# Kernel tuning notes

Hardware: AMD Instinct MI355X
Metric: run time of the kernel (lower is better)

The kernel has to match this reference:

```python
import jax, jax.numpy as jnp
import numpy as np

D_MODEL = 1024
NUM_HEADS = 16
HEAD_DIM = D_MODEL // NUM_HEADS

def setup_inputs() -> dict:
    key = jax.random.key(0)
    ks = jax.random.split(key, 5)
    B, T = 4, 2048
    x = jax.random.normal(ks[0], (B, T, D_MODEL), dtype=jnp.float32)
    s = 1.0 / np.sqrt(D_MODEL)
    W_qkv = jax.random.normal(ks[1], (D_MODEL, 3 * D_MODEL), dtype=jnp.float32) * s
    b_qkv = jnp.zeros((3 * D_MODEL,), dtype=jnp.float32)
    W_out = jax.random.normal(ks[2], (D_MODEL, D_MODEL), dtype=jnp.float32) * s
    b_out = jnp.zeros((D_MODEL,), dtype=jnp.float32)
    return {"x": x, "W_qkv": W_qkv, "b_qkv": b_qkv, "W_out": W_out, "b_out": b_out}

def reference(x, W_qkv, b_qkv, W_out, b_out):
    B, T, C = x.shape
    H, Dh = NUM_HEADS, HEAD_DIM
    qkv = x @ W_qkv + b_qkv                      # [B,T,3C]
    qkv = qkv.reshape(B, T, 3, H, Dh)
    q = jnp.transpose(qkv[:, :, 0], (0, 2, 1, 3))  # [B,H,T,Dh]
    k = jnp.transpose(qkv[:, :, 1], (0, 2, 1, 3))
    v = jnp.transpose(qkv[:, :, 2], (0, 2, 1, 3))
    scores = jnp.einsum('bhqd,bhkd->bhqk', q, k) / jnp.sqrt(jnp.asarray(Dh, x.dtype))
    weights = jax.nn.softmax(scores, axis=-1)
    out = jnp.einsum('bhqk,bhkd->bhqd', weights, v)  # [B,H,T,Dh]
    out = jnp.transpose(out, (0, 2, 1, 3)).reshape(B, T, C)
    return out @ W_out + b_out
```

## Files before the change

kernel.cpp:

```cpp
#include <hip/hip_runtime.h>
#include <stdint.h>

typedef __bf16 bf16x8 __attribute__((ext_vector_type(8)));
typedef float f32x4 __attribute__((ext_vector_type(4)));
typedef float f32x16 __attribute__((ext_vector_type(16)));

static constexpr int BB = 4, TT = 2048, CC = 1024, HH = 16, DH = 64;
static constexpr int MM = BB * TT;
static constexpr int N1 = 3 * CC;
static constexpr int KK = CC;

__device__ __forceinline__ unsigned short f2bf(float f) {
  uint32_t u = __builtin_bit_cast(uint32_t, f);
  u += 0x7FFFu + ((u >> 16) & 1u);
  return (unsigned short)(u >> 16);
}

__device__ __forceinline__ void async16(const void* g, void* l) {
  __builtin_amdgcn_global_load_lds((const __attribute__((address_space(1))) void*)g,
                                   (__attribute__((address_space(3))) void*)l, 16, 0, 0);
}

__global__ __launch_bounds__(256) void k_cvt(const float* __restrict__ src,
                                             unsigned short* __restrict__ dst) {
  int i = blockIdx.x * 256 + threadIdx.x;
  const float4* s = (const float4*)src + (size_t)i * 2;
  float4 a = s[0], b = s[1];
  union { unsigned short h[8]; uint4 v; } o;
  o.h[0] = f2bf(a.x); o.h[1] = f2bf(a.y); o.h[2] = f2bf(a.z); o.h[3] = f2bf(a.w);
  o.h[4] = f2bf(b.x); o.h[5] = f2bf(b.y); o.h[6] = f2bf(b.z); o.h[7] = f2bf(b.w);
  ((uint4*)dst)[i] = o.v;
}

__global__ __launch_bounds__(256) void k_tcvt(const float* __restrict__ src,
                                              unsigned short* __restrict__ dst,
                                              int R, int C) {
  __shared__ float tile[32][33];
  int tx = threadIdx.x & 31, ty = threadIdx.x >> 5;
  int c0 = blockIdx.x * 32, r0 = blockIdx.y * 32;
#pragma unroll
  for (int i = 0; i < 4; ++i)
    tile[ty + i * 8][tx] = src[(size_t)(r0 + ty + i * 8) * C + c0 + tx];
  __syncthreads();
#pragma unroll
  for (int i = 0; i < 4; ++i)
    dst[(size_t)(c0 + ty + i * 8) * R + r0 + tx] = f2bf(tile[tx][ty + i * 8]);
}

#define LDA4(Ab, mf, ksl) \
  (*(const bf16x8*)&(Ab)[(wm * 128 + (mf) * 16 + l15) * 64 + \
                         ((((ksl) * 4 + l16) ^ (l15 & 7)) * 8)])
#define LDB4(Bb, nf, ksl) \
  (*(const bf16x8*)&(Bb)[(wn * 32 + (nf) * 16 + l15) * 64 + \
                         ((((ksl) * 4 + l16) ^ (l15 & 7)) * 8)])

struct AF8 { bf16x8 a[8]; };

template <int P, bool LOADB>
__device__ __forceinline__ AF8 phase_pre4(const unsigned short* Ab, const unsigned short* Bb,
                                          int wm, int wn, int l15, int l16, bf16x8* bfr) {
  AF8 f;
#pragma unroll
  for (int mf = 0; mf < 4; ++mf) {
    f.a[mf * 2] = LDA4(Ab, P * 4 + mf, 0);
    f.a[mf * 2 + 1] = LDA4(Ab, P * 4 + mf, 1);
  }
  if (LOADB) {
#pragma unroll
    for (int nf = 0; nf < 2; ++nf) {
      bfr[nf * 2] = LDB4(Bb, nf, 0);
      bfr[nf * 2 + 1] = LDB4(Bb, nf, 1);
    }
  }
  return f;
}

template <int P>
__device__ __forceinline__ void phase_mfma4(const AF8& f, const bf16x8* bfr, f32x4 acc[8][2]) {
#pragma unroll
  for (int mf = 0; mf < 4; ++mf)
#pragma unroll
    for (int nf = 0; nf < 2; ++nf) {
      acc[P * 4 + mf][nf] = __builtin_amdgcn_mfma_f32_16x16x32_bf16(
          f.a[mf * 2], bfr[nf * 2], acc[P * 4 + mf][nf], 0, 0, 0);
      acc[P * 4 + mf][nf] = __builtin_amdgcn_mfma_f32_16x16x32_bf16(
          f.a[mf * 2 + 1], bfr[nf * 2 + 1], acc[P * 4 + mf][nf], 0, 0, 0);
    }
}

#define PHASE4(P, AB, BB_, LOADB, STAGES, WAITS)                      \
  { AF8 f_ = phase_pre4<P, LOADB>(AB, BB_, wm, wn, l15, l16, bfr);    \
    STAGES;                                                           \
    WAITS;                                                            \
    __builtin_amdgcn_s_barrier();                                     \
    asm volatile("s_waitcnt lgkmcnt(0)" ::: "memory");                \
    __builtin_amdgcn_sched_barrier(0);                                \
    __builtin_amdgcn_s_setprio(1);                                    \
    phase_mfma4<P>(f_, bfr, acc);                                     \
    __builtin_amdgcn_s_setprio(0);                                    \
    __builtin_amdgcn_s_barrier(); }

template <int MODE, int NBX>
__global__ __launch_bounds__(512, 2) void k_gemm4(
    const unsigned short* __restrict__ A, const unsigned short* __restrict__ Bt,
    const float* __restrict__ bias, int M, int N, int K,
    unsigned short* __restrict__ qo, unsigned short* __restrict__ ko,
    unsigned short* __restrict__ vo, float* __restrict__ fo) {
  __shared__ __attribute__((aligned(16))) unsigned short lds[49152];
  unsigned short* As0 = lds;
  unsigned short* As1 = lds + 16384;
  unsigned short* Bs0 = lds + 32768;
  unsigned short* Bs1 = lds + 40960;

  const int tid = threadIdx.x;
  const int lane = tid & 63;
  const int w = tid >> 6, wm = w >> 2, wn = w & 3;
  const int l15 = lane & 15, l16 = lane >> 4;

  const int q8 = (int)gridDim.x >> 3;
  const int swz = ((int)blockIdx.x & 7) * q8 + ((int)blockIdx.x >> 3);
  const int m0 = (swz / NBX) * 256, n0 = (swz % NBX) * 128;

  f32x4 acc[8][2] = {};

  const int srow = tid >> 3;
  const int sg = ((tid & 7) ^ (srow & 7)) * 8;
  const int dOff = srow * 64 + (tid & 7) * 8;
  const unsigned short* aBase = A + (size_t)(m0 + srow) * K + sg;
  const unsigned short* bBase = Bt + (size_t)(n0 + srow) * K + sg;

#define STAGE_A(dst, kt, h)                                                          \
  { async16(aBase + (size_t)((h) * 128) * K + (kt) * 64, (dst) + (h) * 8192 + dOff); \
    async16(aBase + (size_t)((h) * 128 + 64) * K + (kt) * 64,                        \
            (dst) + (h) * 8192 + 4096 + dOff); }
#define STAGE_B(dst, kt)                                                             \
  { async16(bBase + (kt) * 64, (dst) + dOff);                                        \
    async16(bBase + (size_t)64 * K + (kt) * 64, (dst) + 4096 + dOff); }

  STAGE_A(As0, 0, 0); STAGE_A(As0, 0, 1);
  STAGE_B(Bs0, 0);
  STAGE_B(Bs1, 1);
  asm volatile("s_waitcnt vmcnt(0)" ::: "memory");
  __builtin_amdgcn_s_barrier();

  const int NITER = K / 128;
#pragma unroll 1
  for (int i = 0; i < NITER; ++i) {
    const bool more = (i + 1 < NITER);
    const int tb = 2 * i + 1, t2k = 2 * i + 2, t3 = 2 * i + 3;
    bf16x8 bfr[4];
    PHASE4(0, As0, Bs0, true,
           { STAGE_A(As1, tb, 0); STAGE_A(As1, tb, 1); }, ((void)0));
    PHASE4(1, As0, Bs0, false,
           { if (more) STAGE_B(Bs0, t2k); },
           { if (more) { asm volatile("s_waitcnt vmcnt(2)" ::: "memory"); }
             else      { asm volatile("s_waitcnt vmcnt(0)" ::: "memory"); } });
    PHASE4(0, As1, Bs1, true,
           { if (more) { STAGE_A(As0, t2k, 0); STAGE_A(As0, t2k, 1); } }, ((void)0));
    PHASE4(1, As1, Bs1, false,
           { if (more) STAGE_B(Bs1, t3); },
           { if (more) { asm volatile("s_waitcnt vmcnt(2)" ::: "memory"); } });
  }

  if (MODE == 0) {
    const int sel = n0 >> 10;
    if (sel < 2) {
      const float qs = (sel == 0) ? 0.180336892f : 1.0f;
      float bj[2];
#pragma unroll
      for (int nf = 0; nf < 2; ++nf) bj[nf] = bias[n0 + wn * 32 + nf * 16 + l15];
#pragma unroll
      for (int mf = 0; mf < 8; ++mf)
#pragma unroll
        for (int nf = 0; nf < 2; ++nf)
#pragma unroll
          for (int r = 0; r < 4; ++r) {
            const int row = wm * 128 + mf * 16 + l16 * 4 + r;
            const int col = wn * 32 + nf * 16 + l15;
            lds[row * 128 + (col >> 6) * 64 +
                ((((col >> 3) & 7) ^ (row & 7)) * 8) + (col & 7)] =
                f2bf((acc[mf][nf][r] + bj[nf]) * qs);
          }
      __syncthreads();
      const int row = tid >> 1, half = tid & 1;
      const int gm = m0 + row, bb2 = gm >> 11, t2 = gm & 2047;
      const int h2 = ((n0 & 1023) >> 6) + half;
      unsigned short* dst = (sel == 0 ? qo : ko) +
          ((size_t)(bb2 * HH + h2) * TT + t2) * DH;
#pragma unroll
      for (int g = 0; g < 8; ++g) {
        bf16x8 v = *(const bf16x8*)&lds[row * 128 + half * 64 + ((g ^ (row & 7)) * 8)];
        *(bf16x8*)&dst[g * 8] = v;
      }
    } else {
#pragma unroll
      for (int mf = 0; mf < 8; ++mf)
#pragma unroll
        for (int nf = 0; nf < 2; ++nf) {
          const int gn = n0 + wn * 32 + nf * 16 + l15;
          const float bj = bias[gn];
          const int h = (gn & 1023) >> 6, d = gn & 63;
          const int gm0 = m0 + wm * 128 + mf * 16 + l16 * 4;
          const int bb2 = gm0 >> 11, t0 = gm0 & 2047;
          union { unsigned short s[4]; uint2 u; } pk;
#pragma unroll
          for (int r = 0; r < 4; ++r) pk.s[r] = f2bf(acc[mf][nf][r] + bj);
          *(uint2*)&vo[((size_t)(bb2 * HH + h) * DH + d) * TT + t0] = pk.u;
        }
    }
  } else {
#pragma unroll
    for (int mf = 0; mf < 8; ++mf)
#pragma unroll
      for (int nf = 0; nf < 2; ++nf) {
        const int gn = n0 + wn * 32 + nf * 16 + l15;
        const float bj = bias[gn];
#pragma unroll
        for (int r = 0; r < 4; ++r) {
          const int gm = m0 + wm * 128 + mf * 16 + l16 * 4 + r;
          fo[(size_t)gm * N + gn] = acc[mf][nf][r] + bj;
        }
      }
  }
#undef STAGE_A
#undef STAGE_B
}

__global__ __launch_bounds__(256, 2) void k_attn(
    const unsigned short* __restrict__ Q,
    const unsigned short* __restrict__ Kx,
    const unsigned short* __restrict__ Vt,
    unsigned short* __restrict__ At,
    float neg16) {
  __shared__ __attribute__((aligned(16))) unsigned short Ks[2][64 * 64];
  __shared__ __attribute__((aligned(16))) unsigned short Vs[2][64 * 64];
  const int tid = threadIdx.x, lane = tid & 63, w = tid >> 6;
  const int l31 = lane & 31, hi5 = lane >> 5;
  const int id = blockIdx.x;
  const int bh = (id & 7) + ((id >> 7) << 3);
  const int qb = (id >> 3) & 15;
  const int q0 = qb * 128 + w * 32;
  const unsigned short* Qp = Q + (size_t)bh * TT * DH;
  const unsigned short* Kp = Kx + (size_t)bh * TT * DH;
  const unsigned short* Vp = Vt + (size_t)bh * DH * TT;

  bf16x8 qf[4];
#pragma unroll
  for (int j = 0; j < 4; ++j)
    qf[j] = *(const bf16x8*)&Qp[(size_t)(q0 + l31) * DH + j * 16 + hi5 * 8];

  f32x16 cinit;
#pragma unroll
  for (int r = 0; r < 16; ++r) cinit[r] = neg16;

  const int srow = tid >> 3;
  const int sg = ((tid & 7) ^ (srow & 7)) * 8;

  float l8[8];
#pragma unroll
  for (int r = 0; r < 8; ++r) l8[r] = 0.f;
  f32x16 oacc[2] = {};

#pragma unroll
  for (int i = 0; i < 2; ++i) {
    async16(Kp + (size_t)(i * 32 + srow) * DH + sg, &Ks[0][i * 2048 + tid * 8]);
    async16(Vp + (size_t)(i * 32 + srow) * TT + sg, &Vs[0][i * 2048 + tid * 8]);
  }
  __syncthreads();

#pragma unroll 2
  for (int kt = 0; kt < TT / 64; ++kt) {
    const int cur = kt & 1;
    if (kt + 1 < TT / 64) {
      const int kv1 = (kt + 1) * 64;
#pragma unroll
      for (int i = 0; i < 2; ++i) {
        async16(Kp + (size_t)(kv1 + i * 32 + srow) * DH + sg,
                &Ks[cur ^ 1][i * 2048 + tid * 8]);
        async16(Vp + (size_t)(i * 32 + srow) * TT + kv1 + sg,
                &Vs[cur ^ 1][i * 2048 + tid * 8]);
      }
    }

    f32x16 sacc[2];
    __builtin_amdgcn_s_setprio(1);
#pragma unroll
    for (int t = 0; t < 2; ++t) {
      bf16x8 kf = *(const bf16x8*)&Ks[cur][(t * 32 + l31) * 64 +
                      ((hi5 ^ (l31 & 7)) * 8)];
      sacc[t] = __builtin_amdgcn_mfma_f32_32x32x16_bf16(kf, qf[0], cinit, 0, 0, 0);
    }
#pragma unroll
    for (int ks16 = 1; ks16 < 4; ++ks16) {
#pragma unroll
      for (int t = 0; t < 2; ++t) {
        bf16x8 kf = *(const bf16x8*)&Ks[cur][(t * 32 + l31) * 64 +
                        (((ks16 * 2 + hi5) ^ (l31 & 7)) * 8)];
        sacc[t] = __builtin_amdgcn_mfma_f32_32x32x16_bf16(kf, qf[ks16], sacc[t], 0, 0, 0);
      }
    }
    __builtin_amdgcn_s_setprio(0);
    asm volatile("" : "+v"(sacc[0]), "+v"(sacc[1]));

#pragma unroll
    for (int t = 0; t < 2; ++t)
#pragma unroll
      for (int r = 0; r < 16; ++r)
        sacc[t][r] = __builtin_amdgcn_exp2f(sacc[t][r]);
#pragma unroll
    for (int r = 0; r < 4; ++r)
      l8[r] += (sacc[0][r] + sacc[0][r + 8]) + (sacc[1][r] + sacc[1][r + 8]);
#pragma unroll
    for (int r = 4; r < 8; ++r)
      l8[r] += (sacc[0][r] + sacc[0][r + 8]) + (sacc[1][r] + sacc[1][r + 8]);

    uint32_t wpk[16];
#pragma unroll
    for (int t = 0; t < 2; ++t) {
      union { __bf16 h[16]; uint32_t u[8]; } pk;
#pragma unroll
      for (int r = 0; r < 16; ++r) pk.h[r] = (__bf16)sacc[t][r];
#pragma unroll
      for (int j = 0; j < 8; ++j) wpk[t * 8 + j] = pk.u[j];
    }
    uint32_t xw[8];
#pragma unroll
    for (int t = 0; t < 2; ++t) {
      xw[t * 4 + 0] = __shfl_xor(hi5 ? wpk[t * 8 + 0] : wpk[t * 8 + 2], 32);
      xw[t * 4 + 1] = __shfl_xor(hi5 ? wpk[t * 8 + 1] : wpk[t * 8 + 3], 32);
      xw[t * 4 + 2] = __shfl_xor(hi5 ? wpk[t * 8 + 4] : wpk[t * 8 + 6], 32);
      xw[t * 4 + 3] = __shfl_xor(hi5 ? wpk[t * 8 + 5] : wpk[t * 8 + 7], 32);
    }

    __builtin_amdgcn_s_setprio(1);
#pragma unroll
    for (int ks = 0; ks < 4; ++ks) {
      const int t = ks >> 1, b = (ks & 1) * 4, o = t * 8, xb = t * 4 + (ks & 1) * 2;
      union { uint32_t u[4]; bf16x8 v; } pu;
      pu.u[0] = hi5 ? xw[xb] : wpk[o + b];
      pu.u[1] = hi5 ? xw[xb + 1] : wpk[o + b + 1];
      pu.u[2] = hi5 ? wpk[o + b + 2] : xw[xb];
      pu.u[3] = hi5 ? wpk[o + b + 3] : xw[xb + 1];
#pragma unroll
      for (int dt = 0; dt < 2; ++dt) {
        bf16x8 vf = *(const bf16x8*)&Vs[cur][(dt * 32 + l31) * 64 +
                        (((ks * 2 + hi5) ^ (l31 & 7)) * 8)];
        oacc[dt] = __builtin_amdgcn_mfma_f32_32x32x16_bf16(vf, pu.v, oacc[dt], 0, 0, 0);
      }
    }
    __builtin_amdgcn_s_setprio(0);
    __syncthreads();
  }

  float l = ((l8[0] + l8[4]) + (l8[1] + l8[5])) +
            ((l8[2] + l8[6]) + (l8[3] + l8[7]));
  l += __shfl_xor(l, 32);

  const float il = 1.0f / l;
  unsigned short* bw = &Ks[0][0] + w * 2048;
#pragma unroll
  for (int dt = 0; dt < 2; ++dt)
#pragma unroll
    for (int j = 0; j < 8; ++j) {
      const int dl = (j & 1) * 2 + (j >> 1) * 8 + hi5 * 4;
      const int d = dt * 32 + dl;
      const uint32_t pk = (uint32_t)f2bf(oacc[dt][2 * j] * il) |
                          ((uint32_t)f2bf(oacc[dt][2 * j + 1] * il) << 16);
      const int g = d >> 3, gi = (d >> 1) & 3;
      *(uint32_t*)&bw[l31 * 64 + ((g ^ (l31 & 7)) * 8) + gi * 2] = pk;
    }
  __syncthreads();
  const int bb = bh >> 4, hd = bh & 15;
#pragma unroll
  for (int i = 0; i < 4; ++i) {
    const int row = i * 8 + (lane >> 3);
    const int g = lane & 7;
    bf16x8 vv = *(const bf16x8*)&bw[row * 64 + ((g ^ (row & 7)) * 8)];
    *(bf16x8*)&At[((size_t)bb * TT + q0 + row) * CC + hd * DH + g * 8] = vv;
  }
}

extern "C" void kernel_launch(void* const* d_in, const int* in_sizes, int n_in,
                              void* d_out, int out_size, void* d_ws, size_t ws_size,
                              hipStream_t stream) {
  const float* x = (const float*)d_in[0];
  const float* Wqkv = (const float*)d_in[1];
  const float* bqkv = (const float*)d_in[2];
  const float* Wout = (const float*)d_in[3];
  const float* bout = (const float*)d_in[4];
  float* out = (float*)d_out;

  char* ws = (char*)d_ws;
  unsigned short* Xb  = (unsigned short*)(ws);
  unsigned short* WqT = (unsigned short*)(ws + (16ull << 20));
  unsigned short* WoT = (unsigned short*)(ws + (22ull << 20));
  unsigned short* Qb  = (unsigned short*)(ws + (24ull << 20));
  unsigned short* Kb  = (unsigned short*)(ws + (40ull << 20));
  unsigned short* Vt  = (unsigned short*)(ws + (56ull << 20));
  unsigned short* At  = (unsigned short*)(ws + (72ull << 20));

  k_cvt<<<dim3((MM * KK) / (256 * 8)), 256, 0, stream>>>(x, Xb);
  k_tcvt<<<dim3(N1 / 32, KK / 32), 256, 0, stream>>>(Wqkv, WqT, KK, N1);
  k_tcvt<<<dim3(CC / 32, KK / 32), 256, 0, stream>>>(Wout, WoT, KK, CC);
  k_gemm4<0, 24><<<dim3((MM / 256) * (N1 / 128)), 512, 0, stream>>>(
      Xb, WqT, bqkv, MM, N1, KK, Qb, Kb, Vt, nullptr);
  k_attn<<<dim3(BB * HH * (TT / 128)), 256, 0, stream>>>(Qb, Kb, Vt, At, -16.0f);
  k_gemm4<1, 8><<<dim3((MM / 256) * (CC / 128)), 512, 0, stream>>>(
      At, WoT, bout, MM, CC, KK, nullptr, nullptr, nullptr, out);
}
```

Measured before the change: 199.8 us.

## Shrink GEMM tiles to 128x128 with 4 warps of 64x64

Both projection GEMMs move from a 256x128 block tile with 8 warps (each 128x32) to a 128x128 block tile with 4 warps (each 64x64). Staging, LDS layout, MFMA loops, wait counts and epilogues are rewritten to match. Each warp's sub-tile becomes square, and the grid doubles, so the out-projection GEMM gets more blocks (512 instead of 256) to fill the CUs. In exchange each block reuses loaded data less and issues more global traffic per FLOP.

Result: faster. 187.3 us (median of 2 runs) (-6.3%).

```diff
diff --git a/kernel.cpp b/kernel.cpp
--- a/kernel.cpp
+++ b/kernel.cpp
@@ -47,97 +47,100 @@
     dst[(size_t)(c0 + ty + i * 8) * R + r0 + tx] = f2bf(tile[tx][ty + i * 8]);
 }
 
-#define LDA4(Ab, mf, ksl) \
-  (*(const bf16x8*)&(Ab)[(wm * 128 + (mf) * 16 + l15) * 64 + \
+
+#define LDA2(Ab, mf, ksl) \
+  (*(const bf16x8*)&(Ab)[(wm * 64 + (mf) * 16 + l15) * 64 + \
                          ((((ksl) * 4 + l16) ^ (l15 & 7)) * 8)])
-#define LDB4(Bb, nf, ksl) \
-  (*(const bf16x8*)&(Bb)[(wn * 32 + (nf) * 16 + l15) * 64 + \
+#define LDB2(Bb, nf, ksl) \
+  (*(const bf16x8*)&(Bb)[(wn * 64 + (nf) * 16 + l15) * 64 + \
                          ((((ksl) * 4 + l16) ^ (l15 & 7)) * 8)])
 
-struct AF8 { bf16x8 a[8]; };
+struct AF4g { bf16x8 a00, a01, a10, a11; };
 
 template <int P, bool LOADB>
-__device__ __forceinline__ AF8 phase_pre4(const unsigned short* Ab, const unsigned short* Bb,
-                                          int wm, int wn, int l15, int l16, bf16x8* bfr) {
-  AF8 f;
-#pragma unroll
-  for (int mf = 0; mf < 4; ++mf) {
-    f.a[mf * 2] = LDA4(Ab, P * 4 + mf, 0);
-    f.a[mf * 2 + 1] = LDA4(Ab, P * 4 + mf, 1);
-  }
+__device__ __forceinline__ AF4g phase_pre2(const unsigned short* Ab, const unsigned short* Bb,
+                                           int wm, int wn, int l15, int l16, bf16x8* bfr) {
+  AF4g f;
+  f.a00 = LDA2(Ab, P * 2, 0);     f.a01 = LDA2(Ab, P * 2, 1);
+  f.a10 = LDA2(Ab, P * 2 + 1, 0); f.a11 = LDA2(Ab, P * 2 + 1, 1);
   if (LOADB) {
 #pragma unroll
-    for (int nf = 0; nf < 2; ++nf) {
-      bfr[nf * 2] = LDB4(Bb, nf, 0);
-      bfr[nf * 2 + 1] = LDB4(Bb, nf, 1);
+    for (int nf = 0; nf < 4; ++nf) {
+      bfr[nf] = LDB2(Bb, nf, 0);
+      bfr[4 + nf] = LDB2(Bb, nf, 1);
     }
   }
   return f;
 }
 
 template <int P>
-__device__ __forceinline__ void phase_mfma4(const AF8& f, const bf16x8* bfr, f32x4 acc[8][2]) {
-#pragma unroll
-  for (int mf = 0; mf < 4; ++mf)
-#pragma unroll
-    for (int nf = 0; nf < 2; ++nf) {
-      acc[P * 4 + mf][nf] = __builtin_amdgcn_mfma_f32_16x16x32_bf16(
-          f.a[mf * 2], bfr[nf * 2], acc[P * 4 + mf][nf], 0, 0, 0);
-      acc[P * 4 + mf][nf] = __builtin_amdgcn_mfma_f32_16x16x32_bf16(
-          f.a[mf * 2 + 1], bfr[nf * 2 + 1], acc[P * 4 + mf][nf], 0, 0, 0);
-    }
-}
-
-#define PHASE4(P, AB, BB_, LOADB, STAGES, WAITS)                      \
-  { AF8 f_ = phase_pre4<P, LOADB>(AB, BB_, wm, wn, l15, l16, bfr);    \
+__device__ __forceinline__ void phase_mfma2(const AF4g& f, const bf16x8* bfr, f32x4 acc[4][4]) {
+#pragma unroll
+  for (int nf = 0; nf < 4; ++nf)
+    acc[P * 2][nf] = __builtin_amdgcn_mfma_f32_16x16x32_bf16(f.a00, bfr[nf], acc[P * 2][nf], 0, 0, 0);
+#pragma unroll
+  for (int nf = 0; nf < 4; ++nf)
+    acc[P * 2][nf] = __builtin_amdgcn_mfma_f32_16x16x32_bf16(f.a01, bfr[4 + nf], acc[P * 2][nf], 0, 0, 0);
+#pragma unroll
+  for (int nf = 0; nf < 4; ++nf)
+    acc[P * 2 + 1][nf] = __builtin_amdgcn_mfma_f32_16x16x32_bf16(f.a10, bfr[nf], acc[P * 2 + 1][nf], 0, 0, 0);
+#pragma unroll
+  for (int nf = 0; nf < 4; ++nf)
+    acc[P * 2 + 1][nf] = __builtin_amdgcn_mfma_f32_16x16x32_bf16(f.a11, bfr[4 + nf], acc[P * 2 + 1][nf], 0, 0, 0);
+}
+
+#define PHASE2(P, AB, BB_, LOADB, STAGES, WAITS)                      \
+  { AF4g f_ = phase_pre2<P, LOADB>(AB, BB_, wm, wn, l15, l16, bfr);   \
     STAGES;                                                           \
     WAITS;                                                            \
     __builtin_amdgcn_s_barrier();                                     \
     asm volatile("s_waitcnt lgkmcnt(0)" ::: "memory");                \
     __builtin_amdgcn_sched_barrier(0);                                \
     __builtin_amdgcn_s_setprio(1);                                    \
-    phase_mfma4<P>(f_, bfr, acc);                                     \
+    phase_mfma2<P>(f_, bfr, acc);                                     \
     __builtin_amdgcn_s_setprio(0);                                    \
     __builtin_amdgcn_s_barrier(); }
 
 template <int MODE, int NBX>
-__global__ __launch_bounds__(512, 2) void k_gemm4(
+__global__ __launch_bounds__(256, 2) void k_gemm2t(
     const unsigned short* __restrict__ A, const unsigned short* __restrict__ Bt,
     const float* __restrict__ bias, int M, int N, int K,
     unsigned short* __restrict__ qo, unsigned short* __restrict__ ko,
     unsigned short* __restrict__ vo, float* __restrict__ fo) {
-  __shared__ __attribute__((aligned(16))) unsigned short lds[49152];
+  __shared__ __attribute__((aligned(16))) unsigned short lds[32768];
   unsigned short* As0 = lds;
-  unsigned short* As1 = lds + 16384;
-  unsigned short* Bs0 = lds + 32768;
-  unsigned short* Bs1 = lds + 40960;
+  unsigned short* As1 = lds + 8192;
+  unsigned short* Bs0 = lds + 16384;
+  unsigned short* Bs1 = lds + 24576;
 
   const int tid = threadIdx.x;
   const int lane = tid & 63;
-  const int w = tid >> 6, wm = w >> 2, wn = w & 3;
+  const int w = tid >> 6, wm = w >> 1, wn = w & 1;
   const int l15 = lane & 15, l16 = lane >> 4;
 
   const int q8 = (int)gridDim.x >> 3;
   const int swz = ((int)blockIdx.x & 7) * q8 + ((int)blockIdx.x >> 3);
-  const int m0 = (swz / NBX) * 256, n0 = (swz % NBX) * 128;
-
-  f32x4 acc[8][2] = {};
+  const int m0 = (swz / NBX) * 128, n0 = (swz % NBX) * 128;
+
+  f32x4 acc[4][4] = {};
 
   const int srow = tid >> 3;
   const int sg = ((tid & 7) ^ (srow & 7)) * 8;
-  const int dOff = srow * 64 + (tid & 7) * 8;
   const unsigned short* aBase = A + (size_t)(m0 + srow) * K + sg;
   const unsigned short* bBase = Bt + (size_t)(n0 + srow) * K + sg;
 
-#define STAGE_A(dst, kt, h)                                                          \
-  { async16(aBase + (size_t)((h) * 128) * K + (kt) * 64, (dst) + (h) * 8192 + dOff); \
-    async16(aBase + (size_t)((h) * 128 + 64) * K + (kt) * 64,                        \
-            (dst) + (h) * 8192 + 4096 + dOff); }
-#define STAGE_B(dst, kt)                                                             \
-  { async16(bBase + (kt) * 64, (dst) + dOff);                                        \
-    async16(bBase + (size_t)64 * K + (kt) * 64, (dst) + 4096 + dOff); }
-
-  STAGE_A(As0, 0, 0); STAGE_A(As0, 0, 1);
+#define STAGE_A(dst, kt)                                                        \
+  { async16(aBase + (size_t)0 * K + (kt) * 64, (dst) + 0 * 2048 + tid * 8);     \
+    async16(aBase + (size_t)32 * K + (kt) * 64, (dst) + 1 * 2048 + tid * 8);    \
+    async16(aBase + (size_t)64 * K + (kt) * 64, (dst) + 2 * 2048 + tid * 8);    \
+    async16(aBase + (size_t)96 * K + (kt) * 64, (dst) + 3 * 2048 + tid * 8); }
+#define STAGE_B(dst, kt)                                                        \
+  { async16(bBase + (size_t)0 * K + (kt) * 64, (dst) + 0 * 2048 + tid * 8);     \
+    async16(bBase + (size_t)32 * K + (kt) * 64, (dst) + 1 * 2048 + tid * 8);    \
+    async16(bBase + (size_t)64 * K + (kt) * 64, (dst) + 2 * 2048 + tid * 8);    \
+    async16(bBase + (size_t)96 * K + (kt) * 64, (dst) + 3 * 2048 + tid * 8); }
+
+  STAGE_A(As0, 0);
   STAGE_B(Bs0, 0);
   STAGE_B(Bs1, 1);
   asm volatile("s_waitcnt vmcnt(0)" ::: "memory");
@@ -148,35 +151,33 @@
   for (int i = 0; i < NITER; ++i) {
     const bool more = (i + 1 < NITER);
     const int tb = 2 * i + 1, t2k = 2 * i + 2, t3 = 2 * i + 3;
-    bf16x8 bfr[4];
-    PHASE4(0, As0, Bs0, true,
-           { STAGE_A(As1, tb, 0); STAGE_A(As1, tb, 1); }, ((void)0));
-    PHASE4(1, As0, Bs0, false,
+    bf16x8 bfr[8];
+    PHASE2(0, As0, Bs0, true,  { STAGE_A(As1, tb); }, ((void)0));
+    PHASE2(1, As0, Bs0, false,
            { if (more) STAGE_B(Bs0, t2k); },
-           { if (more) { asm volatile("s_waitcnt vmcnt(2)" ::: "memory"); }
+           { if (more) { asm volatile("s_waitcnt vmcnt(4)" ::: "memory"); }
              else      { asm volatile("s_waitcnt vmcnt(0)" ::: "memory"); } });
-    PHASE4(0, As1, Bs1, true,
-           { if (more) { STAGE_A(As0, t2k, 0); STAGE_A(As0, t2k, 1); } }, ((void)0));
-    PHASE4(1, As1, Bs1, false,
+    PHASE2(0, As1, Bs1, true,  { if (more) STAGE_A(As0, t2k); }, ((void)0));
+    PHASE2(1, As1, Bs1, false,
            { if (more) STAGE_B(Bs1, t3); },
-           { if (more) { asm volatile("s_waitcnt vmcnt(2)" ::: "memory"); } });
+           { if (more) { asm volatile("s_waitcnt vmcnt(4)" ::: "memory"); } });
   }
 
   if (MODE == 0) {
     const int sel = n0 >> 10;
     if (sel < 2) {
       const float qs = (sel == 0) ? 0.180336892f : 1.0f;
-      float bj[2];
-#pragma unroll
-      for (int nf = 0; nf < 2; ++nf) bj[nf] = bias[n0 + wn * 32 + nf * 16 + l15];
-#pragma unroll
-      for (int mf = 0; mf < 8; ++mf)
-#pragma unroll
-        for (int nf = 0; nf < 2; ++nf)
+      float bj[4];
+#pragma unroll
+      for (int nf = 0; nf < 4; ++nf) bj[nf] = bias[n0 + wn * 64 + nf * 16 + l15];
+#pragma unroll
+      for (int mf = 0; mf < 4; ++mf)
+#pragma unroll
+        for (int nf = 0; nf < 4; ++nf)
 #pragma unroll
           for (int r = 0; r < 4; ++r) {
-            const int row = wm * 128 + mf * 16 + l16 * 4 + r;
-            const int col = wn * 32 + nf * 16 + l15;
+            const int row = wm * 64 + mf * 16 + l16 * 4 + r;
+            const int col = wn * 64 + nf * 16 + l15;
             lds[row * 128 + (col >> 6) * 64 +
                 ((((col >> 3) & 7) ^ (row & 7)) * 8) + (col & 7)] =
                 f2bf((acc[mf][nf][r] + bj[nf]) * qs);
@@ -194,13 +195,13 @@
       }
     } else {
 #pragma unroll
-      for (int mf = 0; mf < 8; ++mf)
-#pragma unroll
-        for (int nf = 0; nf < 2; ++nf) {
-          const int gn = n0 + wn * 32 + nf * 16 + l15;
+      for (int mf = 0; mf < 4; ++mf)
+#pragma unroll
+        for (int nf = 0; nf < 4; ++nf) {
+          const int gn = n0 + wn * 64 + nf * 16 + l15;
           const float bj = bias[gn];
           const int h = (gn & 1023) >> 6, d = gn & 63;
-          const int gm0 = m0 + wm * 128 + mf * 16 + l16 * 4;
+          const int gm0 = m0 + wm * 64 + mf * 16 + l16 * 4;
           const int bb2 = gm0 >> 11, t0 = gm0 & 2047;
           union { unsigned short s[4]; uint2 u; } pk;
 #pragma unroll
@@ -210,14 +211,14 @@
     }
   } else {
 #pragma unroll
-    for (int mf = 0; mf < 8; ++mf)
-#pragma unroll
-      for (int nf = 0; nf < 2; ++nf) {
-        const int gn = n0 + wn * 32 + nf * 16 + l15;
+    for (int mf = 0; mf < 4; ++mf)
+#pragma unroll
+      for (int nf = 0; nf < 4; ++nf) {
+        const int gn = n0 + wn * 64 + nf * 16 + l15;
         const float bj = bias[gn];
 #pragma unroll
         for (int r = 0; r < 4; ++r) {
-          const int gm = m0 + wm * 128 + mf * 16 + l16 * 4 + r;
+          const int gm = m0 + wm * 64 + mf * 16 + l16 * 4 + r;
           fo[(size_t)gm * N + gn] = acc[mf][nf][r] + bj;
         }
       }
@@ -402,9 +403,9 @@
   k_cvt<<<dim3((MM * KK) / (256 * 8)), 256, 0, stream>>>(x, Xb);
   k_tcvt<<<dim3(N1 / 32, KK / 32), 256, 0, stream>>>(Wqkv, WqT, KK, N1);
   k_tcvt<<<dim3(CC / 32, KK / 32), 256, 0, stream>>>(Wout, WoT, KK, CC);
-  k_gemm4<0, 24><<<dim3((MM / 256) * (N1 / 128)), 512, 0, stream>>>(
+  k_gemm2t<0, 24><<<dim3((MM / 128) * (N1 / 128)), 256, 0, stream>>>(
       Xb, WqT, bqkv, MM, N1, KK, Qb, Kb, Vt, nullptr);
   k_attn<<<dim3(BB * HH * (TT / 128)), 256, 0, stream>>>(Qb, Kb, Vt, At, -16.0f);
-  k_gemm4<1, 8><<<dim3((MM / 256) * (CC / 128)), 512, 0, stream>>>(
+  k_gemm2t<1, 8><<<dim3((MM / 128) * (CC / 128)), 256, 0, stream>>>(
       At, WoT, bout, MM, CC, KK, nullptr, nullptr, nullptr, out);
 }
```
